# Optimization experiments

Measured on AMD Instinct MI355X. Metric: run time of the kernel, lower is better.

The kernel has to match this reference:

```python
import jax, jax.numpy as jnp
import numpy as np

B, S, D_IN, D_OUT = 8, 2048, 1024, 64

def setup_inputs() -> dict:
    key = jax.random.key(0)
    ks = jax.random.split(key, 6)
    return {
        "inputs_for_keys": jax.random.normal(ks[0], (B, S, D_IN), jnp.float32),
        "inputs_for_values": jax.random.normal(ks[1], (B, S, D_IN), jnp.float32),
        "inputs_for_queries": jax.random.normal(ks[2], (B, S, D_IN), jnp.float32),
        "K": jax.random.normal(ks[3], (D_IN, D_OUT), jnp.float32) * (1.0 / np.sqrt(D_IN)),
        "V": jax.random.normal(ks[4], (D_IN, D_OUT), jnp.float32) * (1.0 / np.sqrt(D_IN)),
        "Q": jax.random.normal(ks[5], (D_IN, D_OUT), jnp.float32) * (1.0 / np.sqrt(D_IN)),
    }

def reference(inputs_for_keys, inputs_for_values, inputs_for_queries, K, V, Q):
    # Project to per-head key/value/query spaces: [B, S, D_OUT]
    keys = jnp.einsum('bsd,de->bse', inputs_for_keys, K)
    values = jnp.einsum('bsd,de->bse', inputs_for_values, V)
    queries = jnp.einsum('bsd,de->bse', inputs_for_queries, Q)
    d_k = keys.shape[-1]
    # Scaled dot-product scores: [B, Sq, Sk]
    score = jnp.einsum('bqe,bke->bqk', queries, keys) / jnp.sqrt(jnp.float32(d_k))
    # Causal mask: -inf strictly above the diagonal (query i attends to keys <= i)
    sq, sk = score.shape[1], score.shape[2]
    causal = jnp.triu(jnp.full((sq, sk), -jnp.inf, dtype=score.dtype), k=1)
    score = score + causal[None, :, :]
    weights = jax.nn.softmax(score, axis=-1)
    # Attention output: [B, Sq, D_OUT]
    return jnp.einsum('bqk,bke->bqe', weights, values)
```

## Files before the change

kernel.cpp:

```cpp
#include <hip/hip_runtime.h>
#include <stdint.h>

#define BB   8
#define SS   2048
#define DIN  1024
#define DOUT 64

typedef __bf16 bf16_t;
typedef __bf16 bf16x4 __attribute__((ext_vector_type(4)));
typedef __bf16 bf16x8 __attribute__((ext_vector_type(8)));
typedef float  f32x4  __attribute__((ext_vector_type(4)));
typedef unsigned int u32x4 __attribute__((ext_vector_type(4)));

#define LOG2E 1.44269504088896f

__device__ __forceinline__ void load_lds16(const void* g, void* l) {
    __builtin_amdgcn_global_load_lds(
        (const __attribute__((address_space(1))) void*)g,
        (__attribute__((address_space(3))) void*)l, 16, 0, 0);
}

__global__ void prep_weights(const float* __restrict__ Kw,
                             const float* __restrict__ Vw,
                             const float* __restrict__ Qw,
                             bf16_t* __restrict__ fw) {
    int proj = blockIdx.x >> 4;
    int seg  = blockIdx.x & 15;
    const float* W = (proj == 0) ? Kw : (proj == 1) ? Vw : Qw;
    float scale = (proj == 2) ? 0.125f : 1.0f;
    bf16_t* out = fw + proj * 65536;
    int base = seg * 4096;
#pragma unroll
    for (int i = 0; i < 16; ++i) {
        int idx  = base + i * 256 + threadIdx.x;
        int j    = idx & 7;
        int lane = (idx >> 3) & 63;
        int nt   = (idx >> 9) & 3;
        int kk   = idx >> 11;
        int k    = kk * 32 + (lane >> 4) * 8 + j;
        int col  = nt * 16 + (lane & 15);
        out[idx] = (bf16_t)(W[k * DOUT + col] * scale);
    }
}

__global__ __launch_bounds__(256) void proj_kernel(
    const float* __restrict__ Xk, const float* __restrict__ Xv,
    const float* __restrict__ Xq, const bf16_t* __restrict__ fw,
    bf16_t* __restrict__ outK, bf16_t* __restrict__ outV,
    bf16_t* __restrict__ outQ) {
    __shared__ __align__(128) char Al[8192];
    __shared__ __align__(128) char Bl[8192];

    int tid  = threadIdx.x;
    int lane = tid & 63;
    int w    = tid >> 6;

    int proj = blockIdx.y;
    const float* X  = (proj == 0) ? Xk : (proj == 1) ? Xv : Xq;
    bf16_t* out     = (proj == 0) ? outK : (proj == 1) ? outV : outQ;
    const bf16_t* fwp = fw + proj * 65536;

    int row0 = blockIdx.x * 32;

    const float* ga = X + (size_t)(row0 + (tid >> 4)) * DIN + ((tid & 15) ^ (tid >> 4)) * 4;
    char* alds0 = Al + (w << 10);
    char* alds1 = Al + 4096 + (w << 10);
    char* blds0 = Bl + (w << 10);
    char* blds1 = Bl + 4096 + (w << 10);

    f32x4 acc0 = (f32x4)(0.0f), acc1 = (f32x4)(0.0f);
    int r   = (w & 1) * 16 + (lane & 15);
    int nt0 = (w >> 1) * 2;

    for (int kt = 0; kt < 16; ++kt) {
        load_lds16(ga + kt * 64,               alds0);
        load_lds16(ga + 16 * DIN + kt * 64,    alds1);
        load_lds16(fwp + kt * 4096 + tid * 8,        blds0);
        load_lds16(fwp + kt * 4096 + 2048 + tid * 8, blds1);
        __syncthreads();

#pragma unroll
        for (int s = 0; s < 2; ++s) {
            int b0 = s * 8 + (lane >> 4) * 2;
            f32x4 lo = *(const f32x4*)(Al + r * 256 + (((b0    ) ^ (lane & 15)) << 4));
            f32x4 hi = *(const f32x4*)(Al + r * 256 + (((b0 + 1) ^ (lane & 15)) << 4));
            bf16x8 af;
            af[0] = (bf16_t)lo[0]; af[1] = (bf16_t)lo[1];
            af[2] = (bf16_t)lo[2]; af[3] = (bf16_t)lo[3];
            af[4] = (bf16_t)hi[0]; af[5] = (bf16_t)hi[1];
            af[6] = (bf16_t)hi[2]; af[7] = (bf16_t)hi[3];
            bf16x8 bf0 = *(const bf16x8*)(Bl + s * 4096 + nt0 * 1024 + lane * 16);
            bf16x8 bf1 = *(const bf16x8*)(Bl + s * 4096 + (nt0 + 1) * 1024 + lane * 16);
            acc0 = __builtin_amdgcn_mfma_f32_16x16x32_bf16(af, bf0, acc0, 0, 0, 0);
            acc1 = __builtin_amdgcn_mfma_f32_16x16x32_bf16(af, bf1, acc1, 0, 0, 0);
        }
        __syncthreads();
    }

#pragma unroll
    for (int j = 0; j < 4; ++j) {
        int orow = row0 + (w & 1) * 16 + (lane >> 4) * 4 + j;
        out[(size_t)orow * DOUT + nt0 * 16 + (lane & 15)]       = (bf16_t)acc0[j];
        out[(size_t)orow * DOUT + (nt0 + 1) * 16 + (lane & 15)] = (bf16_t)acc1[j];
    }
}

__global__ __launch_bounds__(256) void attn_kernel(
    const bf16_t* __restrict__ Kp, const bf16_t* __restrict__ Vp,
    const bf16_t* __restrict__ Qp, float* __restrict__ out) {
    __shared__ __align__(16) bf16_t Klds[64 * 64];
    __shared__ __align__(16) bf16_t Vlds[64 * 64];
    __shared__ __align__(16) bf16_t Plds[4][16 * 64];

    int tid   = threadIdx.x;
    int lane  = tid & 63;
    int w     = tid >> 6;
    int qtile = blockIdx.x;
    int batch = blockIdx.y;

    const bf16_t* Kb = Kp + (size_t)batch * SS * DOUT;
    const bf16_t* Vb = Vp + (size_t)batch * SS * DOUT;
    const bf16_t* Qb = Qp + (size_t)batch * SS * DOUT;

    bf16x8 aq[2];
    {
        int r = qtile * 64 + w * 16 + (lane & 15);
        const bf16_t* qp = Qb + (size_t)r * DOUT + (lane >> 4) * 8;
        aq[0] = *(const bf16x8*)(qp);
        aq[1] = *(const bf16x8*)(qp + 32);
    }

    float m[4], lsum[4];
    f32x4 acc[4];
#pragma unroll
    for (int r = 0; r < 4; ++r) { m[r] = -1e30f; lsum[r] = 0.0f; }
#pragma unroll
    for (int nt = 0; nt < 4; ++nt) acc[nt] = (f32x4)(0.0f);

    int ntiles = qtile + 1;
    for (int j = 0; j < ntiles; ++j) {
        __syncthreads();
#pragma unroll
        for (int i = 0; i < 2; ++i) {
            int c   = tid + 256 * i;
            int key = c >> 3;
            int d0  = (c & 7) * 8;
            u32x4 v = *(const u32x4*)(Kb + ((size_t)(j * 64 + key)) * DOUT + d0);
            *(u32x4*)((char*)Klds + key * 128 + ((d0 * 2) ^ ((key & 7) << 4))) = v;
        }
#pragma unroll
        for (int i = 0; i < 2; ++i) {
            int c   = tid + 256 * i;
            int key = c >> 3;
            int d0  = (c & 7) * 8;
            bf16x8 v = *(const bf16x8*)(Vb + ((size_t)(j * 64 + key)) * DOUT + d0);
#pragma unroll
            for (int jj = 0; jj < 8; ++jj) {
                int d = d0 + jj;
                *(bf16_t*)((char*)Vlds + d * 128 + ((key * 2) ^ ((d & 7) << 4))) = v[jj];
            }
        }
        __syncthreads();

        f32x4 sfr[4];
#pragma unroll
        for (int nt = 0; nt < 4; ++nt) sfr[nt] = (f32x4)(0.0f);
#pragma unroll
        for (int kk = 0; kk < 2; ++kk) {
            int d0 = kk * 32 + (lane >> 4) * 8;
#pragma unroll
            for (int nt = 0; nt < 4; ++nt) {
                int key = nt * 16 + (lane & 15);
                bf16x8 bk = *(const bf16x8*)((char*)Klds + key * 128 +
                                             ((d0 * 2) ^ ((key & 7) << 4)));
                sfr[nt] = __builtin_amdgcn_mfma_f32_16x16x32_bf16(aq[kk], bk, sfr[nt], 0, 0, 0);
            }
        }

        if (j == qtile) {
#pragma unroll
            for (int nt = 0; nt < 4; ++nt) {
                int key = nt * 16 + (lane & 15);
#pragma unroll
                for (int r = 0; r < 4; ++r) {
                    int q = w * 16 + (lane >> 4) * 4 + r;
                    if (key > q) sfr[nt][r] = -1e30f;
                }
            }
        }

        float pf[4][4];
#pragma unroll
        for (int r = 0; r < 4; ++r) {
            float mx = fmaxf(fmaxf(sfr[0][r], sfr[1][r]), fmaxf(sfr[2][r], sfr[3][r]));
            mx = fmaxf(mx, __shfl_xor(mx, 1));
            mx = fmaxf(mx, __shfl_xor(mx, 2));
            mx = fmaxf(mx, __shfl_xor(mx, 4));
            mx = fmaxf(mx, __shfl_xor(mx, 8));
            float mn = fmaxf(m[r], mx);
            float scale = exp2f((m[r] - mn) * LOG2E);
            m[r] = mn;
            float rs = 0.0f;
#pragma unroll
            for (int nt = 0; nt < 4; ++nt) {
                float p = exp2f((sfr[nt][r] - mn) * LOG2E);
                pf[nt][r] = p;
                rs += p;
            }
            rs += __shfl_xor(rs, 1);
            rs += __shfl_xor(rs, 2);
            rs += __shfl_xor(rs, 4);
            rs += __shfl_xor(rs, 8);
            lsum[r] = lsum[r] * scale + rs;
#pragma unroll
            for (int nt = 0; nt < 4; ++nt) acc[nt][r] *= scale;
        }

#pragma unroll
        for (int nt = 0; nt < 4; ++nt) {
            int key = nt * 16 + (lane & 15);
#pragma unroll
            for (int r = 0; r < 4; ++r) {
                int q = (lane >> 4) * 4 + r;
                *(bf16_t*)((char*)&Plds[w][0] + q * 128 +
                           ((key * 2) ^ ((q & 7) << 4))) = (bf16_t)pf[nt][r];
            }
        }
        __syncthreads();

#pragma unroll
        for (int kk = 0; kk < 2; ++kk) {
            int k0 = kk * 32 + (lane >> 4) * 8;
            int q  = lane & 15;
            bf16x8 ap = *(const bf16x8*)((char*)&Plds[w][0] + q * 128 +
                                         ((k0 * 2) ^ ((q & 7) << 4)));
#pragma unroll
            for (int nt = 0; nt < 4; ++nt) {
                int d = nt * 16 + (lane & 15);
                bf16x8 bv = *(const bf16x8*)((char*)Vlds + d * 128 +
                                             ((k0 * 2) ^ ((d & 7) << 4)));
                acc[nt] = __builtin_amdgcn_mfma_f32_16x16x32_bf16(ap, bv, acc[nt], 0, 0, 0);
            }
        }
    }

    float* ob = out + ((size_t)batch * SS + qtile * 64 + w * 16) * DOUT;
#pragma unroll
    for (int nt = 0; nt < 4; ++nt) {
#pragma unroll
        for (int r = 0; r < 4; ++r) {
            int q = (lane >> 4) * 4 + r;
            int d = nt * 16 + (lane & 15);
            ob[(size_t)q * DOUT + d] = acc[nt][r] / lsum[r];
        }
    }
}

extern "C" void kernel_launch(void* const* d_in, const int* in_sizes, int n_in,
                              void* d_out, int out_size, void* d_ws, size_t ws_size,
                              hipStream_t stream) {
    const float* Xk = (const float*)d_in[0];
    const float* Xv = (const float*)d_in[1];
    const float* Xq = (const float*)d_in[2];
    const float* Kw = (const float*)d_in[3];
    const float* Vw = (const float*)d_in[4];
    const float* Qw = (const float*)d_in[5];

    bf16_t* Kp = (bf16_t*)d_ws;
    bf16_t* Vp = Kp + (size_t)BB * SS * DOUT;
    bf16_t* Qp = Vp + (size_t)BB * SS * DOUT;
    bf16_t* fw = Qp + (size_t)BB * SS * DOUT;

    prep_weights<<<dim3(48), dim3(256), 0, stream>>>(Kw, Vw, Qw, fw);
    proj_kernel<<<dim3(512, 3), dim3(256), 0, stream>>>(Xk, Xv, Xq, fw, Kp, Vp, Qp);
    attn_kernel<<<dim3(32, 8), dim3(256), 0, stream>>>(Kp, Vp, Qp, (float*)d_out);
}
```

Measured before the change: 109.7 us.

## Split long causal query tiles across blocks, transpose V, read K/V directly

The projection kernel now writes V transposed (d-major per batch), staged through LDS. The attention kernel drops the shared K/V staging and its block barriers and reads K and transposed V fragments straight from global memory per wave. The later 16 query tiles, which have the most key tiles, are split into two halves handled by separate blocks, and a new combine kernel merges them with the usual max/sum rescaling. This targets causal load imbalance and the low block count, at the cost of an extra launch, partial-result traffic and uncached redundant global reads of K/V across waves.

```diff
diff --git a/kernel.cpp b/kernel.cpp
--- a/kernel.cpp
+++ b/kernel.cpp
@@ -46,7 +46,7 @@
 __global__ __launch_bounds__(256) void proj_kernel(
     const float* __restrict__ Xk, const float* __restrict__ Xv,
     const float* __restrict__ Xq, const bf16_t* __restrict__ fw,
-    bf16_t* __restrict__ outK, bf16_t* __restrict__ outV,
+    bf16_t* __restrict__ outK, bf16_t* __restrict__ outVT,
     bf16_t* __restrict__ outQ) {
     __shared__ __align__(128) char Al[8192];
     __shared__ __align__(128) char Bl[8192];
@@ -57,7 +57,7 @@
 
     int proj = blockIdx.y;
     const float* X  = (proj == 0) ? Xk : (proj == 1) ? Xv : Xq;
-    bf16_t* out     = (proj == 0) ? outK : (proj == 1) ? outV : outQ;
+    bf16_t* out     = (proj == 0) ? outK : (proj == 1) ? outVT : outQ;
     const bf16_t* fwp = fw + proj * 65536;
 
     int row0 = blockIdx.x * 32;
@@ -97,37 +97,72 @@
         __syncthreads();
     }
 
-#pragma unroll
-    for (int j = 0; j < 4; ++j) {
-        int orow = row0 + (w & 1) * 16 + (lane >> 4) * 4 + j;
-        out[(size_t)orow * DOUT + nt0 * 16 + (lane & 15)]       = (bf16_t)acc0[j];
-        out[(size_t)orow * DOUT + (nt0 + 1) * 16 + (lane & 15)] = (bf16_t)acc1[j];
+    if (proj != 1) {
+#pragma unroll
+        for (int j = 0; j < 4; ++j) {
+            int orow = row0 + (w & 1) * 16 + (lane >> 4) * 4 + j;
+            out[(size_t)orow * DOUT + nt0 * 16 + (lane & 15)]       = (bf16_t)acc0[j];
+            out[(size_t)orow * DOUT + (nt0 + 1) * 16 + (lane & 15)] = (bf16_t)acc1[j];
+        }
+    } else {
+#pragma unroll
+        for (int j = 0; j < 4; ++j) {
+            int row = (w & 1) * 16 + (lane >> 4) * 4 + j;
+            int c0  = nt0 * 16 + (lane & 15);
+            int c1  = c0 + 16;
+            *(bf16_t*)(Al + row * 128 + ((c0 * 2) ^ ((row & 7) << 4))) = (bf16_t)acc0[j];
+            *(bf16_t*)(Al + row * 128 + ((c1 * 2) ^ ((row & 7) << 4))) = (bf16_t)acc1[j];
+        }
+        __syncthreads();
+        int b  = row0 >> 11;
+        int s0 = row0 & 2047;
+        int sl = tid & 31;
+        int d0 = (tid >> 5) * 8;
+        bf16_t vals[8];
+#pragma unroll
+        for (int j = 0; j < 8; ++j)
+            vals[j] = *(const bf16_t*)(Al + sl * 128 + (((d0 + j) * 2) ^ ((sl & 7) << 4)));
+#pragma unroll
+        for (int j = 0; j < 8; ++j)
+            out[(size_t)b * (DOUT * SS) + (size_t)(d0 + j) * SS + s0 + sl] = vals[j];
     }
 }
 
 __global__ __launch_bounds__(256) void attn_kernel(
-    const bf16_t* __restrict__ Kp, const bf16_t* __restrict__ Vp,
-    const bf16_t* __restrict__ Qp, float* __restrict__ out) {
-    __shared__ __align__(16) bf16_t Klds[64 * 64];
-    __shared__ __align__(16) bf16_t Vlds[64 * 64];
-    __shared__ __align__(16) bf16_t Plds[4][16 * 64];
-
-    int tid   = threadIdx.x;
-    int lane  = tid & 63;
-    int w     = tid >> 6;
-    int qtile = blockIdx.x;
-    int batch = blockIdx.y;
-
-    const bf16_t* Kb = Kp + (size_t)batch * SS * DOUT;
-    const bf16_t* Vb = Vp + (size_t)batch * SS * DOUT;
-    const bf16_t* Qb = Qp + (size_t)batch * SS * DOUT;
-
-    bf16x8 aq[2];
+    const bf16_t* __restrict__ Kp, const bf16_t* __restrict__ VpT,
+    const bf16_t* __restrict__ Qp, float* __restrict__ out,
+    float* __restrict__ Opart, float* __restrict__ Oml, int split) {
+    __shared__ __align__(16) char Plds[4][2048];
+
+    int tid  = threadIdx.x;
+    int lane = tid & 63;
+    int w    = tid >> 6;
+    int idx  = blockIdx.x;
+    int b    = blockIdx.y;
+
+    int qt, t0, t1, half = 0;
+    bool partial;
+    if (!split || idx < 16) { qt = idx; t0 = 0; t1 = qt + 1; partial = false; }
+    else {
+        int e = idx - 16;
+        qt   = 16 + (e >> 1);
+        half = e & 1;
+        int T = qt + 1, h = (T + 1) >> 1;
+        t0 = half ? h : 0;
+        t1 = half ? T : h;
+        partial = true;
+    }
+
+    const bf16_t* Kb = Kp  + (size_t)b * SS * DOUT;
+    const bf16_t* Vb = VpT + (size_t)b * DOUT * SS;
+    const bf16_t* Qb = Qp  + (size_t)b * SS * DOUT;
+
+    bf16x8 aq0, aq1;
     {
-        int r = qtile * 64 + w * 16 + (lane & 15);
-        const bf16_t* qp = Qb + (size_t)r * DOUT + (lane >> 4) * 8;
-        aq[0] = *(const bf16x8*)(qp);
-        aq[1] = *(const bf16x8*)(qp + 32);
+        int rq = qt * 64 + w * 16 + (lane & 15);
+        const bf16_t* qp = Qb + (size_t)rq * DOUT + (lane >> 4) * 8;
+        aq0 = *(const bf16x8*)(qp);
+        aq1 = *(const bf16x8*)(qp + 32);
     }
 
     float m[4], lsum[4];
@@ -137,31 +172,9 @@
 #pragma unroll
     for (int nt = 0; nt < 4; ++nt) acc[nt] = (f32x4)(0.0f);
 
-    int ntiles = qtile + 1;
-    for (int j = 0; j < ntiles; ++j) {
-        __syncthreads();
-#pragma unroll
-        for (int i = 0; i < 2; ++i) {
-            int c   = tid + 256 * i;
-            int key = c >> 3;
-            int d0  = (c & 7) * 8;
-            u32x4 v = *(const u32x4*)(Kb + ((size_t)(j * 64 + key)) * DOUT + d0);
-            *(u32x4*)((char*)Klds + key * 128 + ((d0 * 2) ^ ((key & 7) << 4))) = v;
-        }
-#pragma unroll
-        for (int i = 0; i < 2; ++i) {
-            int c   = tid + 256 * i;
-            int key = c >> 3;
-            int d0  = (c & 7) * 8;
-            bf16x8 v = *(const bf16x8*)(Vb + ((size_t)(j * 64 + key)) * DOUT + d0);
-#pragma unroll
-            for (int jj = 0; jj < 8; ++jj) {
-                int d = d0 + jj;
-                *(bf16_t*)((char*)Vlds + d * 128 + ((key * 2) ^ ((d & 7) << 4))) = v[jj];
-            }
-        }
-        __syncthreads();
-
+    char* Pw = &Plds[w][0];
+
+    for (int t = t0; t < t1; ++t) {
         f32x4 sfr[4];
 #pragma unroll
         for (int nt = 0; nt < 4; ++nt) sfr[nt] = (f32x4)(0.0f);
@@ -171,13 +184,13 @@
 #pragma unroll
             for (int nt = 0; nt < 4; ++nt) {
                 int key = nt * 16 + (lane & 15);
-                bf16x8 bk = *(const bf16x8*)((char*)Klds + key * 128 +
-                                             ((d0 * 2) ^ ((key & 7) << 4)));
-                sfr[nt] = __builtin_amdgcn_mfma_f32_16x16x32_bf16(aq[kk], bk, sfr[nt], 0, 0, 0);
-            }
-        }
-
-        if (j == qtile) {
+                bf16x8 bk = *(const bf16x8*)(Kb + (size_t)(t * 64 + key) * DOUT + d0);
+                sfr[nt] = __builtin_amdgcn_mfma_f32_16x16x32_bf16(
+                              kk == 0 ? aq0 : aq1, bk, sfr[nt], 0, 0, 0);
+            }
+        }
+
+        if (t == qt) {
 #pragma unroll
             for (int nt = 0; nt < 4; ++nt) {
                 int key = nt * 16 + (lane & 15);
@@ -222,37 +235,89 @@
 #pragma unroll
             for (int r = 0; r < 4; ++r) {
                 int q = (lane >> 4) * 4 + r;
-                *(bf16_t*)((char*)&Plds[w][0] + q * 128 +
-                           ((key * 2) ^ ((q & 7) << 4))) = (bf16_t)pf[nt][r];
-            }
-        }
-        __syncthreads();
+                *(bf16_t*)(Pw + q * 128 + ((key * 2) ^ ((q & 7) << 4))) = (bf16_t)pf[nt][r];
+            }
+        }
 
 #pragma unroll
         for (int kk = 0; kk < 2; ++kk) {
             int k0 = kk * 32 + (lane >> 4) * 8;
             int q  = lane & 15;
-            bf16x8 ap = *(const bf16x8*)((char*)&Plds[w][0] + q * 128 +
-                                         ((k0 * 2) ^ ((q & 7) << 4)));
+            bf16x8 ap = *(const bf16x8*)(Pw + q * 128 + ((k0 * 2) ^ ((q & 7) << 4)));
 #pragma unroll
             for (int nt = 0; nt < 4; ++nt) {
                 int d = nt * 16 + (lane & 15);
-                bf16x8 bv = *(const bf16x8*)((char*)Vlds + d * 128 +
-                                             ((k0 * 2) ^ ((d & 7) << 4)));
+                bf16x8 bv = *(const bf16x8*)(Vb + (size_t)d * SS + t * 64 + k0);
                 acc[nt] = __builtin_amdgcn_mfma_f32_16x16x32_bf16(ap, bv, acc[nt], 0, 0, 0);
             }
         }
     }
 
-    float* ob = out + ((size_t)batch * SS + qtile * 64 + w * 16) * DOUT;
-#pragma unroll
-    for (int nt = 0; nt < 4; ++nt) {
-#pragma unroll
-        for (int r = 0; r < 4; ++r) {
-            int q = (lane >> 4) * 4 + r;
-            int d = nt * 16 + (lane & 15);
-            ob[(size_t)q * DOUT + d] = acc[nt][r] / lsum[r];
-        }
+    if (!partial) {
+        float* ob = out + ((size_t)b * SS + qt * 64 + w * 16) * DOUT;
+#pragma unroll
+        for (int nt = 0; nt < 4; ++nt)
+#pragma unroll
+            for (int r = 0; r < 4; ++r) {
+                int q = (lane >> 4) * 4 + r;
+                int d = nt * 16 + (lane & 15);
+                ob[(size_t)q * DOUT + d] = acc[nt][r] / lsum[r];
+            }
+    } else {
+        size_t pbase = (((size_t)b * 16 + (qt - 16)) * 2 + half);
+        float* Op = Opart + pbase * 4096;
+        float* Ml = Oml   + pbase * 128;
+#pragma unroll
+        for (int nt = 0; nt < 4; ++nt)
+#pragma unroll
+            for (int r = 0; r < 4; ++r) {
+                int row = w * 16 + (lane >> 4) * 4 + r;
+                Op[row * 64 + nt * 16 + (lane & 15)] = acc[nt][r];
+            }
+        if ((lane & 15) == 0) {
+#pragma unroll
+            for (int r = 0; r < 4; ++r) {
+                int row = w * 16 + (lane >> 4) * 4 + r;
+                Ml[row * 2]     = m[r];
+                Ml[row * 2 + 1] = lsum[r];
+            }
+        }
+    }
+}
+
+__global__ __launch_bounds__(256) void attn_combine(
+    const float* __restrict__ Opart, const float* __restrict__ Oml,
+    float* __restrict__ out) {
+    int qt  = 16 + blockIdx.x;
+    int b   = blockIdx.y;
+    int tid = threadIdx.x;
+    int row = tid >> 2;
+    int cb  = (tid & 3) * 16;
+
+    size_t base = ((size_t)b * 16 + (qt - 16)) * 2;
+    const float* O0 = Opart + base * 4096;
+    const float* O1 = O0 + 4096;
+    const float* M0 = Oml + base * 128;
+    const float* M1 = M0 + 128;
+
+    float m0 = M0[row * 2], l0 = M0[row * 2 + 1];
+    float m1 = M1[row * 2], l1 = M1[row * 2 + 1];
+    float mm = fmaxf(m0, m1);
+    float e0 = exp2f((m0 - mm) * LOG2E);
+    float e1 = exp2f((m1 - mm) * LOG2E);
+    float li = 1.0f / (l0 * e0 + l1 * e1);
+
+    const float* p0 = O0 + row * 64 + cb;
+    const float* p1 = O1 + row * 64 + cb;
+    float* ob = out + ((size_t)b * SS + qt * 64 + row) * DOUT + cb;
+#pragma unroll
+    for (int i = 0; i < 4; ++i) {
+        f32x4 a = *(const f32x4*)(p0 + i * 4);
+        f32x4 c = *(const f32x4*)(p1 + i * 4);
+        f32x4 o;
+#pragma unroll
+        for (int j = 0; j < 4; ++j) o[j] = (a[j] * e0 + c[j] * e1) * li;
+        *(f32x4*)(ob + i * 4) = o;
     }
 }
 
@@ -266,12 +331,21 @@
     const float* Vw = (const float*)d_in[4];
     const float* Qw = (const float*)d_in[5];
 
-    bf16_t* Kp = (bf16_t*)d_ws;
-    bf16_t* Vp = Kp + (size_t)BB * SS * DOUT;
-    bf16_t* Qp = Vp + (size_t)BB * SS * DOUT;
-    bf16_t* fw = Qp + (size_t)BB * SS * DOUT;
+    bf16_t* Kp  = (bf16_t*)d_ws;
+    bf16_t* VpT = Kp  + (size_t)BB * SS * DOUT;
+    bf16_t* Qp  = VpT + (size_t)BB * SS * DOUT;
+    bf16_t* fw  = Qp  + (size_t)BB * SS * DOUT;
+    char*   pend = (char*)(fw + 3 * 65536);
+    float*  Opart = (float*)pend;
+    float*  Oml   = Opart + (size_t)8 * 16 * 2 * 4096;
+
+    size_t need = (size_t)((char*)(Oml + 8 * 16 * 2 * 128) - (char*)d_ws);
+    int split = (ws_size >= need) ? 1 : 0;
 
     prep_weights<<<dim3(48), dim3(256), 0, stream>>>(Kw, Vw, Qw, fw);
-    proj_kernel<<<dim3(512, 3), dim3(256), 0, stream>>>(Xk, Xv, Xq, fw, Kp, Vp, Qp);
-    attn_kernel<<<dim3(32, 8), dim3(256), 0, stream>>>(Kp, Vp, Qp, (float*)d_out);
-}
+    proj_kernel<<<dim3(512, 3), dim3(256), 0, stream>>>(Xk, Xv, Xq, fw, Kp, VpT, Qp);
+    attn_kernel<<<dim3(split ? 48 : 32, 8), dim3(256), 0, stream>>>(
+        Kp, VpT, Qp, (float*)d_out, Opart, Oml, split);
+    if (split)
+        attn_combine<<<dim3(16, 8), dim3(256), 0, stream>>>(Opart, Oml, (float*)d_out);
+}
```

Result: no change. 107.7 us (median of 2 runs) (-1.8%).
